# Performance work log

Hardware: AMD Instinct MI355X
Metric: run time of the kernel (lower is better)

The kernel has to match this reference:

```python
import jax, jax.numpy as jnp
import numpy as np

DIM = 1024
HEADS = 16
HIDDEN = 4096
EPS = 1e-5


def layernorm(x, w, b):
    mu = jnp.mean(x, axis=-1, keepdims=True)
    var = jnp.var(x, axis=-1, keepdims=True)
    return (x - mu) * jax.lax.rsqrt(var + EPS) * w + b


def setup_inputs() -> dict:
    key = jax.random.key(0)
    ks = jax.random.split(key, 12)
    s = lambda fan_in: 1.0 / np.sqrt(fan_in)
    return {
        "x": jax.random.normal(ks[0], (8, 1024, DIM), dtype=jnp.float32),
        "norm1_w": jnp.ones((DIM,), jnp.float32),
        "norm1_b": jnp.zeros((DIM,), jnp.float32),
        "qkv_w": jax.random.uniform(ks[1], (3 * DIM, DIM), jnp.float32, -s(DIM), s(DIM)),
        "proj_w": jax.random.uniform(ks[2], (DIM, DIM), jnp.float32, -s(DIM), s(DIM)),
        "proj_b": jax.random.uniform(ks[3], (DIM,), jnp.float32, -s(DIM), s(DIM)),
        "norm2_w": jnp.ones((DIM,), jnp.float32),
        "norm2_b": jnp.zeros((DIM,), jnp.float32),
        "fc1_w": jax.random.uniform(ks[4], (HIDDEN, DIM), jnp.float32, -s(DIM), s(DIM)),
        "fc1_b": jax.random.uniform(ks[5], (HIDDEN,), jnp.float32, -s(DIM), s(DIM)),
        "fc2_w": jax.random.uniform(ks[6], (DIM, HIDDEN), jnp.float32, -s(HIDDEN), s(HIDDEN)),
        "fc2_b": jax.random.uniform(ks[7], (DIM,), jnp.float32, -s(HIDDEN), s(HIDDEN)),
    }


def reference(x, norm1_w, norm1_b, qkv_w, proj_w, proj_b,
              norm2_w, norm2_b, fc1_w, fc1_b, fc2_w, fc2_b):
    B, N, C = x.shape
    hd = C // HEADS
    scale = hd ** -0.5

    # ---- attention branch ----
    xn = layernorm(x, norm1_w, norm1_b)
    qkv_tmp = jnp.einsum('bnc,oc->bno', xn, qkv_w)          # [B,N,3C]
    qkv = qkv_tmp.reshape(B, N, 3, HEADS, hd).transpose(2, 0, 3, 1, 4)
    q, k, v = qkv[0], qkv[1], qkv[2]                         # [B,H,N,hd]
    qkv_out = qkv_tmp.reshape(B, N, 3, C).transpose(2, 0, 1, 3)
    attn = jnp.einsum('bhnd,bhmd->bhnm', q, k) * scale       # [B,H,N,N]
    attn = jax.nn.softmax(attn, axis=-1)
    ao = jnp.einsum('bhnm,bhmd->bhnd', attn, v)              # [B,H,N,hd]
    ao = ao.transpose(0, 2, 1, 3).reshape(B, N, C)
    attn_out = jnp.einsum('bnc,oc->bno', ao, proj_w) + proj_b
    x = x + attn_out

    # ---- mlp branch ----
    xn2 = layernorm(x, norm2_w, norm2_b)
    h = jnp.einsum('bnc,hc->bnh', xn2, fc1_w) + fc1_b
    h = jax.nn.gelu(h, approximate=False)
    hidden_out = jnp.einsum('bnh,ch->bnc', h, fc2_w) + fc2_b
    x = x + hidden_out
    return (x, (qkv_out[0], qkv_out[1], qkv_out[2]), hidden_out)
```

## Files before the change

kernel.cpp:

```cpp
#include <hip/hip_runtime.h>
#include <hip/hip_bf16.h>

typedef __attribute__((ext_vector_type(8))) __bf16 bf16x8;
typedef __attribute__((ext_vector_type(4))) float f32x4;
typedef unsigned short u16;
typedef unsigned int u32;

#define TOK 8192
#define C_DIM 1024
#define OUT_SEC 8388608

__device__ __forceinline__ u16 f2bf(float f) {
  return __builtin_bit_cast(u16, __float2bfloat16(f));
}

__device__ __forceinline__ void gl_lds16(const void* g, void* l) {
  __builtin_amdgcn_global_load_lds(
      (__attribute__((address_space(1))) void*)const_cast<void*>(g),
      (__attribute__((address_space(3))) void*)l, 16, 0, 0);
}

__device__ __forceinline__ float gelu_f(float x) {
  float y = 0.7978845608f * (x + 0.044715f * x * x * x);
  y = fminf(fmaxf(y, -15.f), 15.f);
  float e = __expf(2.0f * y);
  float th = (e - 1.0f) / (e + 1.0f);
  return 0.5f * x * (1.0f + th);
}

__global__ __launch_bounds__(256) void cvt_kernel(const float* __restrict__ in,
                                                  u16* __restrict__ out, int n4) {
  int i = blockIdx.x * blockDim.x + threadIdx.x;
  if (i >= n4) return;
  float4 v = reinterpret_cast<const float4*>(in)[i];
  alignas(8) u16 pk[4];
  pk[0] = f2bf(v.x); pk[1] = f2bf(v.y); pk[2] = f2bf(v.z); pk[3] = f2bf(v.w);
  reinterpret_cast<uint2*>(out)[i] = *reinterpret_cast<uint2*>(pk);
}

__global__ __launch_bounds__(256) void ln_kernel(const float* __restrict__ x,
                                                 const float* __restrict__ w,
                                                 const float* __restrict__ b,
                                                 u16* __restrict__ out) {
  const int row = blockIdx.x;
  const int t = threadIdx.x;
  const float* xr = x + (size_t)row * C_DIM;
  float4 v = reinterpret_cast<const float4*>(xr)[t];
  float s = v.x + v.y + v.z + v.w;
  float ss = v.x * v.x + v.y * v.y + v.z * v.z + v.w * v.w;
#pragma unroll
  for (int off = 1; off < 64; off <<= 1) {
    s += __shfl_xor(s, off, 64);
    ss += __shfl_xor(ss, off, 64);
  }
  __shared__ float red[8];
  const int wv = t >> 6;
  if ((t & 63) == 0) { red[wv] = s; red[4 + wv] = ss; }
  __syncthreads();
  s = red[0] + red[1] + red[2] + red[3];
  ss = red[4] + red[5] + red[6] + red[7];
  const float mu = s * (1.0f / C_DIM);
  const float var = ss * (1.0f / C_DIM) - mu * mu;
  const float rstd = rsqrtf(var + 1e-5f);
  float4 w4 = reinterpret_cast<const float4*>(w)[t];
  float4 b4 = reinterpret_cast<const float4*>(b)[t];
  alignas(8) u16 pk[4];
  pk[0] = f2bf((v.x - mu) * rstd * w4.x + b4.x);
  pk[1] = f2bf((v.y - mu) * rstd * w4.y + b4.y);
  pk[2] = f2bf((v.z - mu) * rstd * w4.z + b4.z);
  pk[3] = f2bf((v.w - mu) * rstd * w4.w + b4.w);
  reinterpret_cast<uint2*>(out + (size_t)row * C_DIM)[t] = *reinterpret_cast<uint2*>(pk);
}

__global__ __launch_bounds__(256) void vtrans_kernel(const float* __restrict__ vsrc,
                                                     u16* __restrict__ vt) {
  const int bh = blockIdx.x, nt = blockIdx.y;
  const int b = bh >> 4, h = bh & 15;
  const int t = threadIdx.x;
  __shared__ u16 T[64][65];
#pragma unroll
  for (int p = 0; p < 4; ++p) {
    const int idx = p * 256 + t;
    const int n = idx >> 4, d4 = (idx & 15) * 4;
    float4 x4 = *reinterpret_cast<const float4*>(
        vsrc + (size_t)(b * 1024 + nt * 64 + n) * 1024 + h * 64 + d4);
    T[d4 + 0][n] = f2bf(x4.x);
    T[d4 + 1][n] = f2bf(x4.y);
    T[d4 + 2][n] = f2bf(x4.z);
    T[d4 + 3][n] = f2bf(x4.w);
  }
  __syncthreads();
  const int d = t >> 2, ns = (t & 3) * 16;
  u16* dst = vt + (size_t)bh * 65536 + (size_t)d * 1024 + nt * 64 + ns;
  alignas(16) u16 tmp[16];
#pragma unroll
  for (int i = 0; i < 16; ++i) tmp[i] = T[d][ns + i];
  reinterpret_cast<uint4*>(dst)[0] = reinterpret_cast<uint4*>(tmp)[0];
  reinterpret_cast<uint4*>(dst)[1] = reinterpret_cast<uint4*>(tmp)[1];
}

enum { EPI8_QKV = 0, EPI8_FC1 = 1 };

#define MFMA_Q(BASE)                                                        \
  _Pragma("unroll") for (int nf = 0; nf < 4; ++nf) {                        \
    _Pragma("unroll") for (int mf = 0; mf < 4; ++mf)                        \
        acc[(BASE) + mf][nf] = __builtin_amdgcn_mfma_f32_16x16x32_bf16(     \
            af[mf], bfr[nf], acc[(BASE) + mf][nf], 0, 0, 0);                \
  }

template <int EPI>
__global__ __launch_bounds__(512, 2) void gemm8(
    const u16* __restrict__ A, const u16* __restrict__ Bw,
    const float* __restrict__ bias,
    float* __restrict__ out, u16* __restrict__ h1, u16* __restrict__ h2,
    int K) {
  extern __shared__ char smem[];
  const int t = threadIdx.x, lane = t & 63, wid = t >> 6;
  const int wm = wid >> 2, wn = wid & 3;

  const int nwg = gridDim.x;
  int lin = blockIdx.x;
  lin = (lin & 7) * (nwg >> 3) + (lin >> 3);
  const int brow0 = (lin & 31) * 256;
  const int bcol0 = (lin >> 5) * 256;

  const int NT = K >> 6;

  f32x4 zero = {0.f, 0.f, 0.f, 0.f};
  f32x4 acc[8][4];
#pragma unroll
  for (int m = 0; m < 8; ++m)
#pragma unroll
    for (int n = 0; n < 4; ++n) acc[m][n] = zero;

  const int src_slot = ((t & 3) ^ ((t >> 3) & 3)) * 8;
  const int srow = t >> 2;
  auto stage = [&](int buf, int mat, int ks, int ktile) {
    const u16* G = mat ? Bw : A;
    const int gr0 = mat ? bcol0 : brow0;
    const int k0 = ktile * 64 + ks * 32 + src_slot;
    char* dst = smem + ((buf << 16) | (mat << 15) | (ks << 14));
#pragma unroll
    for (int i = 0; i < 2; ++i)
      gl_lds16(G + (size_t)(gr0 + i * 128 + srow) * K + k0, dst + i * 8192 + t * 16);
  };

  const int swz16 = (((lane >> 4) ^ ((lane >> 1) & 3)) << 4);
  const int l15 = lane & 15;

  stage(0, 0, 0, 0);
  stage(0, 1, 0, 0);
  stage(0, 0, 1, 0);
  stage(0, 1, 1, 0);
  asm volatile("s_waitcnt vmcnt(4)" ::: "memory");
  __builtin_amdgcn_s_barrier();

  for (int tt = 0; tt < NT; ++tt) {
    char* As_ = smem + ((tt & 1) << 16);
    char* Bs_ = As_ + 32768;
    const int nbuf = (tt & 1) ^ 1;
    const bool pf = (tt + 1 < NT);
    bf16x8 af[4], bfr[4];

    auto LDA = [&](int MH, int KK) {
#pragma unroll
      for (int mf = 0; mf < 4; ++mf)
        af[mf] = *reinterpret_cast<const bf16x8*>(
            As_ + KK * 16384 + (wm * 128 + MH * 64 + mf * 16 + l15) * 64 + swz16);
    };
    auto LDB = [&](int KK) {
#pragma unroll
      for (int nf = 0; nf < 4; ++nf)
        bfr[nf] = *reinterpret_cast<const bf16x8*>(
            Bs_ + KK * 16384 + (wn * 64 + nf * 16 + l15) * 64 + swz16);
    };

    LDB(0);
    LDA(0, 0);
    if (pf) stage(nbuf, 0, 0, tt + 1);
    __builtin_amdgcn_s_barrier();
    asm volatile("s_waitcnt lgkmcnt(0)" ::: "memory");
    __builtin_amdgcn_sched_barrier(0);
    __builtin_amdgcn_s_setprio(1);
    MFMA_Q(0)
    __builtin_amdgcn_s_setprio(0);
    __builtin_amdgcn_s_barrier();

    LDA(1, 0);
    if (pf) {
      stage(nbuf, 1, 0, tt + 1);
      asm volatile("s_waitcnt vmcnt(4)" ::: "memory");
    } else {
      asm volatile("s_waitcnt vmcnt(0)" ::: "memory");
    }
    __builtin_amdgcn_s_barrier();
    asm volatile("s_waitcnt lgkmcnt(0)" ::: "memory");
    __builtin_amdgcn_sched_barrier(0);
    __builtin_amdgcn_s_setprio(1);
    MFMA_Q(4)
    __builtin_amdgcn_s_setprio(0);
    __builtin_amdgcn_s_barrier();

    LDB(1);
    LDA(1, 1);
    if (pf) stage(nbuf, 0, 1, tt + 1);
    __builtin_amdgcn_s_barrier();
    asm volatile("s_waitcnt lgkmcnt(0)" ::: "memory");
    __builtin_amdgcn_sched_barrier(0);
    __builtin_amdgcn_s_setprio(1);
    MFMA_Q(4)
    __builtin_amdgcn_s_setprio(0);
    __builtin_amdgcn_s_barrier();

    LDA(0, 1);
    if (pf) {
      stage(nbuf, 1, 1, tt + 1);
      asm volatile("s_waitcnt vmcnt(4)" ::: "memory");
    }
    __builtin_amdgcn_s_barrier();
    asm volatile("s_waitcnt lgkmcnt(0)" ::: "memory");
    __builtin_amdgcn_sched_barrier(0);
    __builtin_amdgcn_s_setprio(1);
    MFMA_Q(0)
    __builtin_amdgcn_s_setprio(0);
    __builtin_amdgcn_s_barrier();
  }

  const int rb = brow0 + wm * 128;
  const int cb = bcol0 + wn * 64;
#pragma unroll
  for (int m = 0; m < 8; ++m) {
#pragma unroll
    for (int n = 0; n < 4; ++n) {
      const int c = cb + n * 16 + l15;
#pragma unroll
      for (int j = 0; j < 4; ++j) {
        const int r = rb + m * 16 + (lane >> 4) * 4 + j;
        float v = acc[m][n][j];
        if constexpr (EPI == EPI8_QKV) {
          const int sec = c >> 10, cc = c & 1023;
          out[(size_t)sec * OUT_SEC + (size_t)r * 1024 + cc] = v;
          const size_t boff =
              (((size_t)(r >> 10) * 16 + (cc >> 6)) * 1024 + (r & 1023)) * 64 + (cc & 63);
          if (sec == 0) h1[boff] = f2bf(v * 0.18033688f);
          else if (sec == 1) h2[boff] = f2bf(v);
        } else {
          v += bias[c];
          h1[(size_t)r * 4096 + c] = f2bf(gelu_f(v));
        }
      }
    }
  }
}

enum { EPIN_PROJ = 0, EPIN_FC2 = 1 };

template <int EPI>
__global__ __launch_bounds__(512, 1) void gemm8n(
    const u16* __restrict__ A, const u16* __restrict__ Bw,
    const float* __restrict__ bias, const float* resid,
    float* out, float* out2_f, int K) {
  extern __shared__ char smem[];
  const int t = threadIdx.x, lane = t & 63, wid = t >> 6;
  const int wm = wid >> 2, wn = wid & 3;

  const int nwg = gridDim.x;
  int lin = blockIdx.x;
  lin = (lin & 7) * (nwg >> 3) + (lin >> 3);
  const int brow0 = (lin & 63) * 128;
  const int bcol0 = (lin >> 6) * 256;

  const int NT = K >> 6;

  f32x4 zero = {0.f, 0.f, 0.f, 0.f};
  f32x4 acc[4][4];
#pragma unroll
  for (int m = 0; m < 4; ++m)
#pragma unroll
    for (int n = 0; n < 4; ++n) acc[m][n] = zero;

  const int src_slot = ((t & 3) ^ ((t >> 3) & 3)) * 8;
  const int srow = t >> 2;
  auto stage_all = [&](char* dst, int ktile) {
#pragma unroll
    for (int ks = 0; ks < 2; ++ks) {
      const int k0 = ktile * 64 + ks * 32 + src_slot;
      gl_lds16(A + (size_t)(brow0 + srow) * K + k0, dst + ks * 8192 + t * 16);
    }
#pragma unroll
    for (int ks = 0; ks < 2; ++ks) {
      const int k0 = ktile * 64 + ks * 32 + src_slot;
      char* db = dst + 16384 + ks * 16384;
#pragma unroll
      for (int i = 0; i < 2; ++i)
        gl_lds16(Bw + (size_t)(bcol0 + i * 128 + srow) * K + k0, db + i * 8192 + t * 16);
    }
  };

  const int swz16 = (((lane >> 4) ^ ((lane >> 1) & 3)) << 4);
  const int l15 = lane & 15;

  char* bcur = smem;
  char* bnxt = smem + 49152;
  char* bspr = smem + 98304;

  stage_all(bcur, 0);
  stage_all(bnxt, 1);
  asm volatile("s_waitcnt vmcnt(6)" ::: "memory");
  __builtin_amdgcn_s_barrier();

  for (int tt = 0; tt < NT; ++tt) {
    const bool pf2 = (tt + 2 < NT);
    bf16x8 af[4], bfr[4];

    auto LDA = [&](int KK) {
#pragma unroll
      for (int mf = 0; mf < 4; ++mf)
        af[mf] = *reinterpret_cast<const bf16x8*>(
            bcur + KK * 8192 + (wm * 64 + mf * 16 + l15) * 64 + swz16);
    };
    auto LDB = [&](int KK) {
#pragma unroll
      for (int nf = 0; nf < 4; ++nf)
        bfr[nf] = *reinterpret_cast<const bf16x8*>(
            bcur + 16384 + KK * 16384 + (wn * 64 + nf * 16 + l15) * 64 + swz16);
    };

    LDA(0);
    LDB(0);
    if (pf2) stage_all(bspr, tt + 2);
    __builtin_amdgcn_s_barrier();
    asm volatile("s_waitcnt lgkmcnt(0)" ::: "memory");
    __builtin_amdgcn_sched_barrier(0);
    __builtin_amdgcn_s_setprio(1);
    MFMA_Q(0)
    __builtin_amdgcn_s_setprio(0);
    __builtin_amdgcn_s_barrier();

    LDA(1);
    LDB(1);
    if (pf2) {
      asm volatile("s_waitcnt vmcnt(6)" ::: "memory");
    } else {
      asm volatile("s_waitcnt vmcnt(0)" ::: "memory");
    }
    __builtin_amdgcn_s_barrier();
    asm volatile("s_waitcnt lgkmcnt(0)" ::: "memory");
    __builtin_amdgcn_sched_barrier(0);
    __builtin_amdgcn_s_setprio(1);
    MFMA_Q(0)
    __builtin_amdgcn_s_setprio(0);
    __builtin_amdgcn_s_barrier();

    char* tmp = bcur;
    bcur = bnxt;
    bnxt = bspr;
    bspr = tmp;
  }

  const int rb = brow0 + wm * 64;
  const int cb = bcol0 + wn * 64;
#pragma unroll
  for (int m = 0; m < 4; ++m) {
#pragma unroll
    for (int n = 0; n < 4; ++n) {
      const int c = cb + n * 16 + l15;
#pragma unroll
      for (int j = 0; j < 4; ++j) {
        const int r = rb + m * 16 + (lane >> 4) * 4 + j;
        float v = acc[m][n][j];
        if constexpr (EPI == EPIN_PROJ) {
          v += bias[c] + resid[(size_t)r * 1024 + c];
          out[(size_t)r * 1024 + c] = v;
        } else {
          v += bias[c];
          out[(size_t)r * 1024 + c] = v;
          out2_f[(size_t)r * 1024 + c] = resid[(size_t)r * 1024 + c] + v;
        }
      }
    }
  }
}

__global__ __launch_bounds__(256) void attn_kernel(const u16* __restrict__ Qb,
                                                   const u16* __restrict__ Kb,
                                                   const u16* __restrict__ Vtb,
                                                   u16* __restrict__ ao) {
  const int orig = blockIdx.y * gridDim.x + blockIdx.x;
  const int wid = (orig & 7) * 256 + (orig >> 3);
  const int bh = wid >> 4;
  const int qt = wid & 15;
  const int b = bh >> 4, h = bh & 15;
  const int t = threadIdx.x, lane = t & 63, wv = t >> 6;
  const int l15 = lane & 15, g = lane >> 4;

  __shared__ u16 Ks[2][4096];
  __shared__ u16 Vs[2][4096];

  const int q0 = qt * 64 + wv * 16;
  bf16x8 qf[2];
#pragma unroll
  for (int c = 0; c < 2; ++c)
    qf[c] = *reinterpret_cast<const bf16x8*>(
        Qb + (size_t)bh * 65536 + (size_t)(q0 + l15) * 64 + c * 32 + g * 8);

  f32x4 zero = {0.f, 0.f, 0.f, 0.f};
  f32x4 accO[4];
#pragma unroll
  for (int nb = 0; nb < 4; ++nb) accO[nb] = zero;
  float m = -1e30f, lrun = 0.f;

  const char* ktile0 = (const char*)(Kb + (size_t)bh * 65536);
  const char* vbase = (const char*)(Vtb + (size_t)bh * 65536);

  auto stage = [&](int buf, int kv0) {
#pragma unroll
    for (int i = 0; i < 2; ++i) {
      const int o = i * 4096 + t * 16;
      const int row = o >> 7, colb = o & 127;
      const int swz = colb ^ ((row & 7) << 4);
      gl_lds16(ktile0 + (size_t)kv0 * 128 + (size_t)row * 128 + swz, (char*)Ks[buf] + o);
      gl_lds16(vbase + (size_t)row * 2048 + (size_t)kv0 * 2 + swz, (char*)Vs[buf] + o);
    }
  };

  stage(0, 0);
  __syncthreads();
  int cur = 0;

  const int a0 = (l15 + ((g & 1) << 5)) << 2;
  const int a1 = a0 + 64;
  const bool up = (lane & 32) != 0;

  for (int tile = 0; tile < 16; ++tile) {
    if (tile < 15) stage(cur ^ 1, (tile + 1) * 64);

    f32x4 sacc[4];
#pragma unroll
    for (int jb = 0; jb < 4; ++jb) sacc[jb] = zero;
#pragma unroll
    for (int jb = 0; jb < 4; ++jb)
#pragma unroll
      for (int c = 0; c < 2; ++c) {
        const int row = jb * 16 + l15;
        const int colb = c * 64 + g * 16;
        bf16x8 kf = *reinterpret_cast<const bf16x8*>(
            (const char*)Ks[cur] + row * 128 + (colb ^ ((row & 7) << 4)));
        sacc[jb] = __builtin_amdgcn_mfma_f32_16x16x32_bf16(kf, qf[c], sacc[jb], 0, 0, 0);
      }

    float mt = sacc[0][0];
#pragma unroll
    for (int jb = 0; jb < 4; ++jb)
#pragma unroll
      for (int r = 0; r < 4; ++r) mt = fmaxf(mt, sacc[jb][r]);
    mt = fmaxf(mt, __shfl_xor(mt, 16, 64));
    mt = fmaxf(mt, __shfl_xor(mt, 32, 64));

    if (!__all(mt <= m + 8.0f)) {
      const float mn = fmaxf(m, mt);
      const float sc = exp2f(m - mn);
      lrun *= sc;
#pragma unroll
      for (int nb = 0; nb < 4; ++nb) accO[nb] *= sc;
      m = mn;
    }

    float rs = 0.f;
#pragma unroll
    for (int jb = 0; jb < 4; ++jb)
#pragma unroll
      for (int r = 0; r < 4; ++r) {
        const float p = exp2f(sacc[jb][r] - m);
        sacc[jb][r] = p;
        rs += p;
      }
    rs += __shfl_xor(rs, 16, 64);
    rs += __shfl_xor(rs, 32, 64);
    lrun += rs;

    int w[4][2];
#pragma unroll
    for (int jb = 0; jb < 4; ++jb) {
      w[jb][0] = (int)((u32)f2bf(sacc[jb][0]) | ((u32)f2bf(sacc[jb][1]) << 16));
      w[jb][1] = (int)((u32)f2bf(sacc[jb][2]) | ((u32)f2bf(sacc[jb][3]) << 16));
    }

#pragma unroll
    for (int c = 0; c < 2; ++c) {
      int lo0 = __builtin_amdgcn_ds_bpermute(a0, w[2 * c][0]);
      int hi0 = __builtin_amdgcn_ds_bpermute(a0, w[2 * c + 1][0]);
      int lo1 = __builtin_amdgcn_ds_bpermute(a0, w[2 * c][1]);
      int hi1 = __builtin_amdgcn_ds_bpermute(a0, w[2 * c + 1][1]);
      int lo2 = __builtin_amdgcn_ds_bpermute(a1, w[2 * c][0]);
      int hi2 = __builtin_amdgcn_ds_bpermute(a1, w[2 * c + 1][0]);
      int lo3 = __builtin_amdgcn_ds_bpermute(a1, w[2 * c][1]);
      int hi3 = __builtin_amdgcn_ds_bpermute(a1, w[2 * c + 1][1]);
      alignas(16) int word[4] = {up ? hi0 : lo0, up ? hi1 : lo1,
                                 up ? hi2 : lo2, up ? hi3 : lo3};
      bf16x8 pfB = *reinterpret_cast<bf16x8*>(word);
#pragma unroll
      for (int nb = 0; nb < 4; ++nb) {
        const int row = nb * 16 + l15;
        const int colb = c * 64 + g * 16;
        bf16x8 vf = *reinterpret_cast<const bf16x8*>(
            (const char*)Vs[cur] + row * 128 + (colb ^ ((row & 7) << 4)));
        accO[nb] = __builtin_amdgcn_mfma_f32_16x16x32_bf16(vf, pfB, accO[nb], 0, 0, 0);
      }
    }

    __syncthreads();
    cur ^= 1;
  }

  const float rl = __builtin_amdgcn_rcpf(lrun);
  u16* dst = ao + (size_t)(b * 1024 + q0 + l15) * 1024 + h * 64 + g * 4;
#pragma unroll
  for (int nb = 0; nb < 4; ++nb) {
    alignas(8) u16 pk[4];
#pragma unroll
    for (int j = 0; j < 4; ++j) pk[j] = f2bf(accO[nb][j] * rl);
    *reinterpret_cast<uint2*>(dst + nb * 16) = *reinterpret_cast<uint2*>(pk);
  }
}

extern "C" void kernel_launch(void* const* d_in, const int* in_sizes, int n_in,
                              void* d_out, int out_size, void* d_ws, size_t ws_size,
                              hipStream_t stream) {
  const float* x      = (const float*)d_in[0];
  const float* n1w    = (const float*)d_in[1];
  const float* n1b    = (const float*)d_in[2];
  const float* qkv_w  = (const float*)d_in[3];
  const float* proj_w = (const float*)d_in[4];
  const float* proj_b = (const float*)d_in[5];
  const float* n2w    = (const float*)d_in[6];
  const float* n2b    = (const float*)d_in[7];
  const float* fc1_w  = (const float*)d_in[8];
  const float* fc1_b  = (const float*)d_in[9];
  const float* fc2_w  = (const float*)d_in[10];
  const float* fc2_b  = (const float*)d_in[11];
  float* out = (float*)d_out;

  u16* wsb    = (u16*)d_ws;
  u16* w_qkv  = wsb;
  u16* w_proj = wsb + 3145728;
  u16* w_fc1  = wsb + 4194304;
  u16* w_fc2  = wsb + 8388608;
  u16* xn     = wsb + 12582912;
  u16* Qb     = wsb + 20971520;
  u16* Kb     = wsb + 29360128;
  u16* Vtw    = wsb + 37748736;
  u16* ao     = wsb + 46137344;
  u16* hbuf   = wsb + 20971520;

  (void)hipFuncSetAttribute((const void*)gemm8<EPI8_QKV>,
                            hipFuncAttributeMaxDynamicSharedMemorySize, 131072);
  (void)hipFuncSetAttribute((const void*)gemm8<EPI8_FC1>,
                            hipFuncAttributeMaxDynamicSharedMemorySize, 131072);
  (void)hipFuncSetAttribute((const void*)gemm8n<EPIN_PROJ>,
                            hipFuncAttributeMaxDynamicSharedMemorySize, 147456);
  (void)hipFuncSetAttribute((const void*)gemm8n<EPIN_FC2>,
                            hipFuncAttributeMaxDynamicSharedMemorySize, 147456);

  cvt_kernel<<<3072, 256, 0, stream>>>(qkv_w, w_qkv, 786432);
  cvt_kernel<<<1024, 256, 0, stream>>>(proj_w, w_proj, 262144);
  cvt_kernel<<<4096, 256, 0, stream>>>(fc1_w, w_fc1, 1048576);
  cvt_kernel<<<4096, 256, 0, stream>>>(fc2_w, w_fc2, 1048576);

  ln_kernel<<<TOK, 256, 0, stream>>>(x, n1w, n1b, xn);
  gemm8<EPI8_QKV><<<384, 512, 131072, stream>>>(
      xn, w_qkv, nullptr, out + OUT_SEC, Qb, Kb, 1024);
  vtrans_kernel<<<dim3(128, 16), 256, 0, stream>>>(out + 3 * (size_t)OUT_SEC, Vtw);
  attn_kernel<<<dim3(128, 16), 256, 0, stream>>>(Qb, Kb, Vtw, ao);
  gemm8n<EPIN_PROJ><<<256, 512, 147456, stream>>>(
      ao, w_proj, proj_b, x, out, nullptr, 1024);
  ln_kernel<<<TOK, 256, 0, stream>>>(out, n2w, n2b, xn);
  gemm8<EPI8_FC1><<<512, 512, 131072, stream>>>(
      xn, w_fc1, fc1_b, nullptr, hbuf, nullptr, 1024);
  gemm8n<EPIN_FC2><<<256, 512, 147456, stream>>>(
      hbuf, w_fc2, fc2_b, out, out + 4 * (size_t)OUT_SEC, out, 4096);
}
```

Baseline: 473.0 us.

## Merge GEMM main-loop phases to overlap LDS fragment loads with MFMA

Both bf16 GEMM main loops now issue the LDS fragment reads for two sub-steps at once, into separate register sets (af/af2, bfr/bfr2). The MFMAs for the first set start after a partial lgkmcnt wait, and the global-to-LDS prefetches are issued together. This halves the number of phases and workgroup barriers per K tile and is meant to hide LDS latency behind matrix work. In exchange it needs more fragment registers, which risks register pressure or spills under the 512-thread, 2-block launch bounds. The hand-tuned waitcnt values also have to stay consistent with the new load ordering.

```diff
diff --git a/kernel.cpp b/kernel.cpp
--- a/kernel.cpp
+++ b/kernel.cpp
@@ -99,14 +99,14 @@
   reinterpret_cast<uint4*>(dst)[1] = reinterpret_cast<uint4*>(tmp)[1];
 }
 
-enum { EPI8_QKV = 0, EPI8_FC1 = 1 };
-
-#define MFMA_Q(BASE)                                                        \
+#define MFMA_T(AF, BF, BASE)                                                \
   _Pragma("unroll") for (int nf = 0; nf < 4; ++nf) {                        \
     _Pragma("unroll") for (int mf = 0; mf < 4; ++mf)                        \
         acc[(BASE) + mf][nf] = __builtin_amdgcn_mfma_f32_16x16x32_bf16(     \
-            af[mf], bfr[nf], acc[(BASE) + mf][nf], 0, 0, 0);                \
-  }
+            AF[mf], BF[nf], acc[(BASE) + mf][nf], 0, 0, 0);                 \
+  }
+
+enum { EPI8_QKV = 0, EPI8_FC1 = 1 };
 
 template <int EPI>
 __global__ __launch_bounds__(512, 2) void gemm8(
@@ -160,12 +160,12 @@
     char* Bs_ = As_ + 32768;
     const int nbuf = (tt & 1) ^ 1;
     const bool pf = (tt + 1 < NT);
-    bf16x8 af[4], bfr[4];
-
-    auto LDA = [&](int MH, int KK) {
+    bf16x8 af[4], af2[4], bfr[4];
+
+    auto LDA = [&](bf16x8* dst8, int MH, int KK) {
 #pragma unroll
       for (int mf = 0; mf < 4; ++mf)
-        af[mf] = *reinterpret_cast<const bf16x8*>(
+        dst8[mf] = *reinterpret_cast<const bf16x8*>(
             As_ + KK * 16384 + (wm * 128 + MH * 64 + mf * 16 + l15) * 64 + swz16);
     };
     auto LDB = [&](int KK) {
@@ -176,53 +176,42 @@
     };
 
     LDB(0);
-    LDA(0, 0);
-    if (pf) stage(nbuf, 0, 0, tt + 1);
-    __builtin_amdgcn_s_barrier();
+    LDA(af, 0, 0);
+    __builtin_amdgcn_sched_barrier(0);
+    LDA(af2, 1, 0);
+    __builtin_amdgcn_sched_barrier(0);
+    if (pf) { stage(nbuf, 0, 0, tt + 1); stage(nbuf, 1, 0, tt + 1); }
+    asm volatile("s_waitcnt lgkmcnt(4)" ::: "memory");
+    __builtin_amdgcn_sched_barrier(0);
+    __builtin_amdgcn_s_setprio(1);
+    MFMA_T(af, bfr, 0)
     asm volatile("s_waitcnt lgkmcnt(0)" ::: "memory");
     __builtin_amdgcn_sched_barrier(0);
-    __builtin_amdgcn_s_setprio(1);
-    MFMA_Q(0)
+    MFMA_T(af2, bfr, 4)
     __builtin_amdgcn_s_setprio(0);
-    __builtin_amdgcn_s_barrier();
-
-    LDA(1, 0);
     if (pf) {
-      stage(nbuf, 1, 0, tt + 1);
       asm volatile("s_waitcnt vmcnt(4)" ::: "memory");
     } else {
       asm volatile("s_waitcnt vmcnt(0)" ::: "memory");
     }
     __builtin_amdgcn_s_barrier();
+
+    LDB(1);
+    LDA(af, 1, 1);
+    __builtin_amdgcn_sched_barrier(0);
+    LDA(af2, 0, 1);
+    __builtin_amdgcn_sched_barrier(0);
+    if (pf) { stage(nbuf, 0, 1, tt + 1); stage(nbuf, 1, 1, tt + 1); }
+    asm volatile("s_waitcnt lgkmcnt(4)" ::: "memory");
+    __builtin_amdgcn_sched_barrier(0);
+    __builtin_amdgcn_s_setprio(1);
+    MFMA_T(af, bfr, 4)
     asm volatile("s_waitcnt lgkmcnt(0)" ::: "memory");
     __builtin_amdgcn_sched_barrier(0);
-    __builtin_amdgcn_s_setprio(1);
-    MFMA_Q(4)
+    MFMA_T(af2, bfr, 0)
     __builtin_amdgcn_s_setprio(0);
-    __builtin_amdgcn_s_barrier();
-
-    LDB(1);
-    LDA(1, 1);
-    if (pf) stage(nbuf, 0, 1, tt + 1);
-    __builtin_amdgcn_s_barrier();
-    asm volatile("s_waitcnt lgkmcnt(0)" ::: "memory");
-    __builtin_amdgcn_sched_barrier(0);
-    __builtin_amdgcn_s_setprio(1);
-    MFMA_Q(4)
-    __builtin_amdgcn_s_setprio(0);
-    __builtin_amdgcn_s_barrier();
-
-    LDA(0, 1);
-    if (pf) {
-      stage(nbuf, 1, 1, tt + 1);
+    if (pf)
       asm volatile("s_waitcnt vmcnt(4)" ::: "memory");
-    }
-    __builtin_amdgcn_s_barrier();
-    asm volatile("s_waitcnt lgkmcnt(0)" ::: "memory");
-    __builtin_amdgcn_sched_barrier(0);
-    __builtin_amdgcn_s_setprio(1);
-    MFMA_Q(0)
-    __builtin_amdgcn_s_setprio(0);
     __builtin_amdgcn_s_barrier();
   }
 
@@ -311,45 +300,41 @@
 
   for (int tt = 0; tt < NT; ++tt) {
     const bool pf2 = (tt + 2 < NT);
-    bf16x8 af[4], bfr[4];
-
-    auto LDA = [&](int KK) {
+    bf16x8 af[4], af2[4], bfr[4], bfr2[4];
+
+    auto LDA = [&](bf16x8* dst8, int KK) {
 #pragma unroll
       for (int mf = 0; mf < 4; ++mf)
-        af[mf] = *reinterpret_cast<const bf16x8*>(
+        dst8[mf] = *reinterpret_cast<const bf16x8*>(
             bcur + KK * 8192 + (wm * 64 + mf * 16 + l15) * 64 + swz16);
     };
-    auto LDB = [&](int KK) {
+    auto LDB = [&](bf16x8* dst8, int KK) {
 #pragma unroll
       for (int nf = 0; nf < 4; ++nf)
-        bfr[nf] = *reinterpret_cast<const bf16x8*>(
+        dst8[nf] = *reinterpret_cast<const bf16x8*>(
             bcur + 16384 + KK * 16384 + (wn * 64 + nf * 16 + l15) * 64 + swz16);
     };
 
-    LDA(0);
-    LDB(0);
+    LDA(af, 0);
+    LDB(bfr, 0);
+    __builtin_amdgcn_sched_barrier(0);
+    LDA(af2, 1);
+    LDB(bfr2, 1);
+    __builtin_amdgcn_sched_barrier(0);
     if (pf2) stage_all(bspr, tt + 2);
-    __builtin_amdgcn_s_barrier();
+    asm volatile("s_waitcnt lgkmcnt(8)" ::: "memory");
+    __builtin_amdgcn_sched_barrier(0);
+    __builtin_amdgcn_s_setprio(1);
+    MFMA_T(af, bfr, 0)
     asm volatile("s_waitcnt lgkmcnt(0)" ::: "memory");
     __builtin_amdgcn_sched_barrier(0);
-    __builtin_amdgcn_s_setprio(1);
-    MFMA_Q(0)
+    MFMA_T(af2, bfr2, 0)
     __builtin_amdgcn_s_setprio(0);
-    __builtin_amdgcn_s_barrier();
-
-    LDA(1);
-    LDB(1);
     if (pf2) {
       asm volatile("s_waitcnt vmcnt(6)" ::: "memory");
     } else {
       asm volatile("s_waitcnt vmcnt(0)" ::: "memory");
     }
-    __builtin_amdgcn_s_barrier();
-    asm volatile("s_waitcnt lgkmcnt(0)" ::: "memory");
-    __builtin_amdgcn_sched_barrier(0);
-    __builtin_amdgcn_s_setprio(1);
-    MFMA_Q(0)
-    __builtin_amdgcn_s_setprio(0);
     __builtin_amdgcn_s_barrier();
 
     char* tmp = bcur;
```

Measured after the change: 440.1 us. 1.07x faster.
